# Kernel optimization log

Measured on AMD Instinct MI355X. Metric: run time of the kernel, lower is better.

## Reference

```python
import jax, jax.numpy as jnp
import numpy as np

KERNEL_MUL = 2.0
KERNEL_NUM = 5


def setup_inputs() -> dict:
    key = jax.random.key(0)
    k1, k2 = jax.random.split(key)
    source = jax.random.normal(k1, (4096, 256), dtype=jnp.float32)
    target = jax.random.normal(k2, (4096, 256), dtype=jnp.float32)
    return {"source": source, "target": target}


def reference(source, target):
    B = source.shape[0]
    total = jnp.concatenate([source, target], axis=0)  # [2N, D]
    n = total.shape[0]
    # Pairwise squared L2 distances via ||a||^2 + ||b||^2 - 2 a.b (same math,
    # avoids the O(n^2 * D) expanded intermediate of the torch code).
    sq = jnp.sum(total * total, axis=-1)  # [2N]
    L2 = sq[:, None] + sq[None, :] - 2.0 * (total @ total.T)  # [2N, 2N]
    L2 = jnp.maximum(L2, 0.0)  # exact distances are non-negative
    # bandwidth uses L2_distance.data in torch -> stop_gradient here
    bandwidth = jax.lax.stop_gradient(jnp.sum(L2)) / (n * n - n)
    bandwidth = bandwidth / (KERNEL_MUL ** (KERNEL_NUM // 2))
    kernels = jnp.zeros_like(L2)
    for i in range(KERNEL_NUM):
        bw = bandwidth * (KERNEL_MUL ** i) + 1e-9
        kernels = kernels + jnp.exp(-L2 / bw)
    xx = jnp.mean(kernels[:B, :B])
    yy = jnp.mean(kernels[B:, B:])
    xy = jnp.mean(kernels[:B, B:])
    yx = jnp.mean(kernels[B:, :B])
    loss = xx + yy - xy - yx  # == mean(XX + YY - XY - YX) since blocks are BxB
    return (loss, jnp.max(L2), xx, yy, xy, yx)
```

## Files before the change

### kernel.cpp

```cpp
#include <hip/hip_runtime.h>
#include <math.h>


constexpr int NTOT  = 8192;
constexpr int BHALF = 4096;
constexpr int DIM   = 256;
constexpr int BM    = 128;

typedef __attribute__((ext_vector_type(8))) short bf16x8;
typedef __attribute__((ext_vector_type(4))) float f32x4;

#define GLOAD_LDS16(gp, lp)                                                      \
    __builtin_amdgcn_global_load_lds(                                            \
        (__attribute__((address_space(1))) const void*)(gp),                     \
        (__attribute__((address_space(3))) void*)(lp), 16, 0, 0)


__device__ __forceinline__ int swz(int row, int byteInRow) {
    return (row * 128 + byteInRow) ^ ((row & 7) << 4);
}

__device__ __forceinline__ unsigned short rne_bf16(float f, float* hf_out) {
    unsigned u = __float_as_uint(f);
    unsigned r = (u + 0x7fffu + ((u >> 16) & 1u)) >> 16;
    *hf_out = __uint_as_float(r << 16);
    return (unsigned short)r;
}

__global__ __launch_bounds__(256) void prep_kernel(
        const float* __restrict__ src, const float* __restrict__ tgt,
        float* __restrict__ sq, double* __restrict__ vcol,
        unsigned short* __restrict__ hi, unsigned short* __restrict__ lo) {
    __shared__ float cs[4][256];
    const int t = threadIdx.x;
    const int w = t >> 6, l = t & 63;
    const int seg = l >> 4;
    const int b8  = (l * 8) & 127;
    float c0 = 0.f, c1 = 0.f, c2 = 0.f, c3 = 0.f;

#pragma unroll
    for (int it = 0; it < 8; ++it) {
        const int row = blockIdx.x * 32 + w * 8 + it;
        const float* p = (row < BHALF) ? src + (size_t)row * DIM
                                       : tgt + (size_t)(row - BHALF) * DIM;
        float4 v = reinterpret_cast<const float4*>(p)[l];
        float s = v.x * v.x + v.y * v.y + v.z * v.z + v.w * v.w;
#pragma unroll
        for (int off = 32; off; off >>= 1) s += __shfl_down(s, off);
        if (l == 0) sq[row] = s;
        c0 += v.x; c1 += v.y; c2 += v.z; c3 += v.w;

        float f[4] = {v.x, v.y, v.z, v.w};
        unsigned hp[2], lp[2];
#pragma unroll
        for (int j = 0; j < 2; ++j) {
            float hf0, hf1;
            unsigned h0 = rne_bf16(f[2*j],   &hf0);
            unsigned h1 = rne_bf16(f[2*j+1], &hf1);
            float d0, d1;
            unsigned l0 = rne_bf16(f[2*j]   - hf0, &d0);
            unsigned l1 = rne_bf16(f[2*j+1] - hf1, &d1);
            hp[j] = h0 | (h1 << 16);
            lp[j] = l0 | (l1 << 16);
        }
        const size_t byteoff = (size_t)row * 512 + seg * 128 + (b8 ^ ((row & 7) << 4));
        *reinterpret_cast<uint2*>((char*)hi + byteoff) = make_uint2(hp[0], hp[1]);
        *reinterpret_cast<uint2*>((char*)lo + byteoff) = make_uint2(lp[0], lp[1]);
    }

    cs[w][l * 4 + 0] = c0; cs[w][l * 4 + 1] = c1;
    cs[w][l * 4 + 2] = c2; cs[w][l * 4 + 3] = c3;
    __syncthreads();
    float tot = cs[0][t] + cs[1][t] + cs[2][t] + cs[3][t];
    atomicAdd(&vcol[t], (double)tot);
}

__global__ void bw_kernel(const float* __restrict__ sq,
                          const double* __restrict__ v,
                          float* __restrict__ bwp) {
    __shared__ double red[256];
    int t = threadIdx.x;
    double s = 0.0;
    for (int i = t; i < NTOT; i += 256) s += (double)sq[i];
    red[t] = s; __syncthreads();
    for (int off = 128; off; off >>= 1) {
        if (t < off) red[t] += red[t + off];
        __syncthreads();
    }
    double S1 = red[0];
    __syncthreads();
    double d = v[t];
    red[t] = d * d; __syncthreads();
    for (int off = 128; off; off >>= 1) {
        if (t < off) red[t] += red[t + off];
        __syncthreads();
    }
    if (t == 0) {
        double V2 = red[0];
        const double n = (double)NTOT;
        double sumL2 = 2.0 * n * S1 - 2.0 * V2;
        *bwp = (float)(sumL2 / (n * n - n) / 4.0);
    }
}

__global__ __launch_bounds__(256) void gram_kernel(
        const unsigned short* __restrict__ hi, const unsigned short* __restrict__ lo,
        const float* __restrict__ sq, const float* __restrict__ bwp,
        double* __restrict__ qsum, int* __restrict__ maxBits) {
    const int bx = blockIdx.x, by = blockIdx.y;
    if (bx < by) return;

    __shared__ alignas(16) char ldsAhi[BM * 128];
    __shared__ alignas(16) char ldsAlo[BM * 128];
    __shared__ alignas(16) char ldsBhi[BM * 128];
    __shared__ alignas(16) char ldsBlo[BM * 128];
    __shared__ double sred[4];
    __shared__ float  mred[4];

    const int i0 = by * BM;
    const int j0 = bx * BM;
    const bool diag = (bx == by);

    const char* Ahi = (const char*)hi + (size_t)i0 * 512;
    const char* Alo = (const char*)lo + (size_t)i0 * 512;
    const char* Bhi = (const char*)hi + (size_t)j0 * 512;
    const char* Blo = (const char*)lo + (size_t)j0 * 512;

    const int t    = threadIdx.x;
    const int lane = t & 63;
    const int w    = t >> 6;
    const int wr   = w >> 1;
    const int wc   = w & 1;
    const int lrow = lane & 15;

    f32x4 acc[4][4] = {};

    for (int seg = 0; seg < 4; ++seg) {
#pragma unroll
        for (int it = 0; it < 4; ++it) {
            const int chunk = it * 4 + w;
            const int o     = chunk * 1024 + lane * 16;
            const int row   = o >> 7;
            const size_t srcoff = (size_t)row * 512 + seg * 128 + (o & 127);
            char* dA = ldsAhi + chunk * 1024;
            char* dB = ldsBhi + chunk * 1024;
            GLOAD_LDS16(Ahi + srcoff, dA);
            GLOAD_LDS16(Alo + srcoff, ldsAlo + chunk * 1024);
            if (!diag) {
                GLOAD_LDS16(Bhi + srcoff, dB);
                GLOAD_LDS16(Blo + srcoff, ldsBlo + chunk * 1024);
            }
        }
        __syncthreads();

        const char* bhbuf = diag ? ldsAhi : ldsBhi;
        const char* blbuf = diag ? ldsAlo : ldsBlo;

#pragma unroll
        for (int ks = 0; ks < 2; ++ks) {
            const int kb = ks * 64 + (lane >> 4) * 16;
            bf16x8 ahi[4], alo[4], bhi[4], blo[4];
#pragma unroll
            for (int mt = 0; mt < 4; ++mt) {
                int off = swz(wr * 64 + mt * 16 + lrow, kb);
                ahi[mt] = *reinterpret_cast<const bf16x8*>(ldsAhi + off);
                alo[mt] = *reinterpret_cast<const bf16x8*>(ldsAlo + off);
            }
#pragma unroll
            for (int nt = 0; nt < 4; ++nt) {
                int off = swz(wc * 64 + nt * 16 + lrow, kb);
                bhi[nt] = *reinterpret_cast<const bf16x8*>(bhbuf + off);
                blo[nt] = *reinterpret_cast<const bf16x8*>(blbuf + off);
            }
#pragma unroll
            for (int mt = 0; mt < 4; ++mt)
#pragma unroll
                for (int nt = 0; nt < 4; ++nt) {
                    acc[mt][nt] = __builtin_amdgcn_mfma_f32_16x16x32_bf16(
                        ahi[mt], bhi[nt], acc[mt][nt], 0, 0, 0);
                    acc[mt][nt] = __builtin_amdgcn_mfma_f32_16x16x32_bf16(
                        ahi[mt], blo[nt], acc[mt][nt], 0, 0, 0);
                    acc[mt][nt] = __builtin_amdgcn_mfma_f32_16x16x32_bf16(
                        alo[mt], bhi[nt], acc[mt][nt], 0, 0, 0);
                }
        }
        __syncthreads();
    }

    const float bw = *bwp;
    float ic[5];
#pragma unroll
    for (int i = 0; i < 5; ++i) ic[i] = -1.0f / (bw * (float)(1 << i) + 1e-9f);

    float m = 0.0f;
    float ksum = 0.0f;
    const int rbase = i0 + wr * 64 + (lane >> 4) * 4;
    const int cbase = j0 + wc * 64 + lrow;
    float sb[4];
#pragma unroll
    for (int nt = 0; nt < 4; ++nt) sb[nt] = sq[cbase + nt * 16];
#pragma unroll
    for (int mt = 0; mt < 4; ++mt) {
        float sa[4];
#pragma unroll
        for (int r = 0; r < 4; ++r) sa[r] = sq[rbase + mt * 16 + r];
#pragma unroll
        for (int nt = 0; nt < 4; ++nt)
#pragma unroll
            for (int r = 0; r < 4; ++r) {
                float l2 = fmaxf(sa[r] + sb[nt] - 2.0f * acc[mt][nt][r], 0.0f);
                m = fmaxf(m, l2);
                ksum += __expf(l2 * ic[0]) + __expf(l2 * ic[1]) + __expf(l2 * ic[2])
                      + __expf(l2 * ic[3]) + __expf(l2 * ic[4]);
            }
    }

    double s = (double)ksum;
#pragma unroll
    for (int off = 32; off; off >>= 1) {
        s += __shfl_down(s, off);
        m  = fmaxf(m, __shfl_down(m, off));
    }
    if ((t & 63) == 0) { sred[w] = s; mred[w] = m; }
    __syncthreads();
    if (t == 0) {
        double st = sred[0] + sred[1] + sred[2] + sred[3];
        float  mt = fmaxf(fmaxf(mred[0], mred[1]), fmaxf(mred[2], mred[3]));
        atomicMax(maxBits, __float_as_int(mt));
        const int q  = (((i0 >= BHALF) ? 2 : 0) | ((j0 >= BHALF) ? 1 : 0));
        const int qT = (((j0 >= BHALF) ? 2 : 0) | ((i0 >= BHALF) ? 1 : 0));
        if (diag) {
            atomicAdd(&qsum[q], st);
        } else if (q == qT) {
            atomicAdd(&qsum[q], 2.0 * st);
        } else {
            atomicAdd(&qsum[q],  st);
            atomicAdd(&qsum[qT], st);
        }
    }
}

__global__ void final_kernel(const double* __restrict__ qsum,
                             const int* __restrict__ maxBits,
                             float* __restrict__ out) {
    const double denom = (double)BHALF * (double)BHALF;
    const double xx = qsum[0] / denom;
    const double xy = qsum[1] / denom;
    const double yx = qsum[2] / denom;
    const double yy = qsum[3] / denom;
    out[0] = (float)(xx + yy - xy - yx);
    out[1] = __int_as_float(*maxBits);
    out[2] = (float)xx;
    out[3] = (float)yy;
    out[4] = (float)xy;
    out[5] = (float)yx;
}

extern "C" void kernel_launch(void* const* d_in, const int* in_sizes, int n_in,
                              void* d_out, int out_size, void* d_ws, size_t ws_size,
                              hipStream_t stream) {
    const float* src = (const float*)d_in[0];
    const float* tgt = (const float*)d_in[1];
    float* out = (float*)d_out;

    double* qsum = (double*)d_ws;
    int*    maxB = (int*)   ((char*)d_ws + 32);
    float*  bwp  = (float*) ((char*)d_ws + 36);
    double* vcol = (double*)((char*)d_ws + 64);
    float*  sq   = (float*) ((char*)d_ws + 2112);
    unsigned short* hi = (unsigned short*)((char*)d_ws + 36864);
    unsigned short* lo = (unsigned short*)((char*)d_ws + 36864 + (size_t)NTOT * DIM * 2);

    hipMemsetAsync(d_ws, 0, 2112, stream);

    prep_kernel<<<NTOT / 32, 256, 0, stream>>>(src, tgt, sq, vcol, hi, lo);
    bw_kernel<<<1, 256, 0, stream>>>(sq, vcol, bwp);

    dim3 grid(NTOT / BM, NTOT / BM);
    gram_kernel<<<grid, 256, 0, stream>>>(hi, lo, sq, bwp, qsum, maxB);

    final_kernel<<<1, 1, 0, stream>>>(qsum, maxB, out);
}
```

Before: 188.2 us.

## Use single bf16 MFMA instead of hi/lo split and launch only triangle tiles

```diff
diff --git a/kernel.cpp b/kernel.cpp
--- a/kernel.cpp
+++ b/kernel.cpp
@@ -20,17 +20,15 @@
     return (row * 128 + byteInRow) ^ ((row & 7) << 4);
 }
 
-__device__ __forceinline__ unsigned short rne_bf16(float f, float* hf_out) {
+__device__ __forceinline__ unsigned short rne_bf16(float f) {
     unsigned u = __float_as_uint(f);
-    unsigned r = (u + 0x7fffu + ((u >> 16) & 1u)) >> 16;
-    *hf_out = __uint_as_float(r << 16);
-    return (unsigned short)r;
+    return (unsigned short)((u + 0x7fffu + ((u >> 16) & 1u)) >> 16);
 }
 
 __global__ __launch_bounds__(256) void prep_kernel(
         const float* __restrict__ src, const float* __restrict__ tgt,
         float* __restrict__ sq, double* __restrict__ vcol,
-        unsigned short* __restrict__ hi, unsigned short* __restrict__ lo) {
+        unsigned short* __restrict__ hi) {
     __shared__ float cs[4][256];
     const int t = threadIdx.x;
     const int w = t >> 6, l = t & 63;
@@ -50,22 +48,10 @@
         if (l == 0) sq[row] = s;
         c0 += v.x; c1 += v.y; c2 += v.z; c3 += v.w;
 
-        float f[4] = {v.x, v.y, v.z, v.w};
-        unsigned hp[2], lp[2];
-#pragma unroll
-        for (int j = 0; j < 2; ++j) {
-            float hf0, hf1;
-            unsigned h0 = rne_bf16(f[2*j],   &hf0);
-            unsigned h1 = rne_bf16(f[2*j+1], &hf1);
-            float d0, d1;
-            unsigned l0 = rne_bf16(f[2*j]   - hf0, &d0);
-            unsigned l1 = rne_bf16(f[2*j+1] - hf1, &d1);
-            hp[j] = h0 | (h1 << 16);
-            lp[j] = l0 | (l1 << 16);
-        }
+        unsigned hp0 = (unsigned)rne_bf16(v.x) | ((unsigned)rne_bf16(v.y) << 16);
+        unsigned hp1 = (unsigned)rne_bf16(v.z) | ((unsigned)rne_bf16(v.w) << 16);
         const size_t byteoff = (size_t)row * 512 + seg * 128 + (b8 ^ ((row & 7) << 4));
-        *reinterpret_cast<uint2*>((char*)hi + byteoff) = make_uint2(hp[0], hp[1]);
-        *reinterpret_cast<uint2*>((char*)lo + byteoff) = make_uint2(lp[0], lp[1]);
+        *reinterpret_cast<uint2*>((char*)hi + byteoff) = make_uint2(hp0, hp1);
     }
 
     cs[w][l * 4 + 0] = c0; cs[w][l * 4 + 1] = c1;
@@ -103,28 +89,29 @@
     }
 }
 
-__global__ __launch_bounds__(256) void gram_kernel(
-        const unsigned short* __restrict__ hi, const unsigned short* __restrict__ lo,
+__global__ __launch_bounds__(256, 4) void gram_kernel(
+        const unsigned short* __restrict__ hi,
         const float* __restrict__ sq, const float* __restrict__ bwp,
         double* __restrict__ qsum, int* __restrict__ maxBits) {
-    const int bx = blockIdx.x, by = blockIdx.y;
-    if (bx < by) return;
-
-    __shared__ alignas(16) char ldsAhi[BM * 128];
-    __shared__ alignas(16) char ldsAlo[BM * 128];
-    __shared__ alignas(16) char ldsBhi[BM * 128];
-    __shared__ alignas(16) char ldsBlo[BM * 128];
+    const int tb = blockIdx.x;
+    const int id = (tb & 7) * 260 + (tb >> 3);
+    int k = 2079 - id;
+    int u = (int)((sqrt((double)(8 * k + 1)) - 1.0) * 0.5);
+    while ((u + 1) * (u + 2) / 2 <= k) ++u;
+    while (u * (u + 1) / 2 > k) --u;
+    const int by = 63 - u;
+    const int bx = 63 - (k - u * (u + 1) / 2);
+    const bool diag = (bx == by);
+
+    __shared__ alignas(16) char ldsA[BM * 128];
+    __shared__ alignas(16) char ldsB[BM * 128];
     __shared__ double sred[4];
     __shared__ float  mred[4];
 
     const int i0 = by * BM;
     const int j0 = bx * BM;
-    const bool diag = (bx == by);
-
     const char* Ahi = (const char*)hi + (size_t)i0 * 512;
-    const char* Alo = (const char*)lo + (size_t)i0 * 512;
     const char* Bhi = (const char*)hi + (size_t)j0 * 512;
-    const char* Blo = (const char*)lo + (size_t)j0 * 512;
 
     const int t    = threadIdx.x;
     const int lane = t & 63;
@@ -142,55 +129,39 @@
             const int o     = chunk * 1024 + lane * 16;
             const int row   = o >> 7;
             const size_t srcoff = (size_t)row * 512 + seg * 128 + (o & 127);
-            char* dA = ldsAhi + chunk * 1024;
-            char* dB = ldsBhi + chunk * 1024;
-            GLOAD_LDS16(Ahi + srcoff, dA);
-            GLOAD_LDS16(Alo + srcoff, ldsAlo + chunk * 1024);
-            if (!diag) {
-                GLOAD_LDS16(Bhi + srcoff, dB);
-                GLOAD_LDS16(Blo + srcoff, ldsBlo + chunk * 1024);
-            }
+            GLOAD_LDS16(Ahi + srcoff, ldsA + chunk * 1024);
+            if (!diag) GLOAD_LDS16(Bhi + srcoff, ldsB + chunk * 1024);
         }
         __syncthreads();
 
-        const char* bhbuf = diag ? ldsAhi : ldsBhi;
-        const char* blbuf = diag ? ldsAlo : ldsBlo;
-
+        const char* bbuf = diag ? ldsA : ldsB;
 #pragma unroll
         for (int ks = 0; ks < 2; ++ks) {
             const int kb = ks * 64 + (lane >> 4) * 16;
-            bf16x8 ahi[4], alo[4], bhi[4], blo[4];
-#pragma unroll
-            for (int mt = 0; mt < 4; ++mt) {
-                int off = swz(wr * 64 + mt * 16 + lrow, kb);
-                ahi[mt] = *reinterpret_cast<const bf16x8*>(ldsAhi + off);
-                alo[mt] = *reinterpret_cast<const bf16x8*>(ldsAlo + off);
-            }
-#pragma unroll
-            for (int nt = 0; nt < 4; ++nt) {
-                int off = swz(wc * 64 + nt * 16 + lrow, kb);
-                bhi[nt] = *reinterpret_cast<const bf16x8*>(bhbuf + off);
-                blo[nt] = *reinterpret_cast<const bf16x8*>(blbuf + off);
-            }
+            bf16x8 a[4], b[4];
 #pragma unroll
             for (int mt = 0; mt < 4; ++mt)
-#pragma unroll
-                for (int nt = 0; nt < 4; ++nt) {
+                a[mt] = *reinterpret_cast<const bf16x8*>(
+                    ldsA + swz(wr * 64 + mt * 16 + lrow, kb));
+#pragma unroll
+            for (int nt = 0; nt < 4; ++nt)
+                b[nt] = *reinterpret_cast<const bf16x8*>(
+                    bbuf + swz(wc * 64 + nt * 16 + lrow, kb));
+#pragma unroll
+            for (int mt = 0; mt < 4; ++mt)
+#pragma unroll
+                for (int nt = 0; nt < 4; ++nt)
                     acc[mt][nt] = __builtin_amdgcn_mfma_f32_16x16x32_bf16(
-                        ahi[mt], bhi[nt], acc[mt][nt], 0, 0, 0);
-                    acc[mt][nt] = __builtin_amdgcn_mfma_f32_16x16x32_bf16(
-                        ahi[mt], blo[nt], acc[mt][nt], 0, 0, 0);
-                    acc[mt][nt] = __builtin_amdgcn_mfma_f32_16x16x32_bf16(
-                        alo[mt], bhi[nt], acc[mt][nt], 0, 0, 0);
-                }
+                        a[mt], b[nt], acc[mt][nt], 0, 0, 0);
         }
         __syncthreads();
     }
 
     const float bw = *bwp;
+    const float L2E = 1.44269504088896340736f;
     float ic[5];
 #pragma unroll
-    for (int i = 0; i < 5; ++i) ic[i] = -1.0f / (bw * (float)(1 << i) + 1e-9f);
+    for (int i = 0; i < 5; ++i) ic[i] = -L2E / (bw * (float)(1 << i) + 1e-9f);
 
     float m = 0.0f;
     float ksum = 0.0f;
@@ -210,8 +181,8 @@
             for (int r = 0; r < 4; ++r) {
                 float l2 = fmaxf(sa[r] + sb[nt] - 2.0f * acc[mt][nt][r], 0.0f);
                 m = fmaxf(m, l2);
-                ksum += __expf(l2 * ic[0]) + __expf(l2 * ic[1]) + __expf(l2 * ic[2])
-                      + __expf(l2 * ic[3]) + __expf(l2 * ic[4]);
+                ksum += exp2f(l2 * ic[0]) + exp2f(l2 * ic[1]) + exp2f(l2 * ic[2])
+                      + exp2f(l2 * ic[3]) + exp2f(l2 * ic[4]);
             }
     }
 
@@ -269,15 +240,11 @@
     double* vcol = (double*)((char*)d_ws + 64);
     float*  sq   = (float*) ((char*)d_ws + 2112);
     unsigned short* hi = (unsigned short*)((char*)d_ws + 36864);
-    unsigned short* lo = (unsigned short*)((char*)d_ws + 36864 + (size_t)NTOT * DIM * 2);
 
     hipMemsetAsync(d_ws, 0, 2112, stream);
 
-    prep_kernel<<<NTOT / 32, 256, 0, stream>>>(src, tgt, sq, vcol, hi, lo);
+    prep_kernel<<<NTOT / 32, 256, 0, stream>>>(src, tgt, sq, vcol, hi);
     bw_kernel<<<1, 256, 0, stream>>>(sq, vcol, bwp);
-
-    dim3 grid(NTOT / BM, NTOT / BM);
-    gram_kernel<<<grid, 256, 0, stream>>>(hi, lo, sq, bwp, qsum, maxB);
-
+    gram_kernel<<<2080, 256, 0, stream>>>(hi, sq, bwp, qsum, maxB);
     final_kernel<<<1, 1, 0, stream>>>(qsum, maxB, out);
 }
```

After: 172.2 us. -8.5%, faster.
